# Kernel tuning notes

Measured on AMD Instinct MI355X. Metric: run time of the kernel, lower is better.

## Reference

```python
import jax, jax.numpy as jnp
import numpy as np

EMBEDDING_DIM = 256
NUM_EMBEDDINGS = 2048
COMMITMENT_COST = 0.25


def setup_inputs() -> dict:
    key = jax.random.key(0)
    k1, k2 = jax.random.split(key)
    inputs = jax.random.normal(k1, (32, EMBEDDING_DIM, 32, 32), dtype=jnp.float32)
    # learned codebook buffer, shape (D, K) as in the torch module
    embedding = jax.random.normal(k2, (EMBEDDING_DIM, NUM_EMBEDDINGS), dtype=jnp.float32)
    return {"inputs": inputs, "embedding": embedding}


def reference(inputs, embedding):
    # Eval-mode forward of VectorQuantizerEMA (EMA buffer updates are
    # training-only side effects and do not affect the returned values).
    B, D, H, W = inputs.shape
    K = embedding.shape[1]
    x = inputs.astype(jnp.float32)
    # (B, D, H, W) -> (N, D), N = B*H*W, clamped as in the source
    flat = jnp.clip(jnp.transpose(x, (0, 2, 3, 1)).reshape(-1, D), -10.0, 10.0)
    # squared L2 distances to every codeword: (N, K)
    distances = (
        jnp.sum(flat * flat, axis=1, keepdims=True)
        + jnp.sum(embedding * embedding, axis=0, keepdims=True)
        - 2.0 * (flat @ embedding)
    )
    encoding_indices = jnp.argmin(distances, axis=1)  # (N,)
    # one-hot @ emb.T is just a gather of codebook columns
    q_flat = jnp.take(embedding.T, encoding_indices, axis=0)  # (N, D)
    quantized = jnp.transpose(q_flat.reshape(B, H, W, D), (0, 3, 1, 2))
    # VQ losses (computed against the un-clamped float inputs, as in torch)
    e_latent_loss = jnp.mean((jax.lax.stop_gradient(quantized) - x) ** 2)
    q_latent_loss = jnp.mean((quantized - jax.lax.stop_gradient(x)) ** 2)
    loss = q_latent_loss + COMMITMENT_COST * e_latent_loss
    # straight-through estimator
    quantized_st = inputs + jax.lax.stop_gradient(quantized - inputs)
    # perplexity from codeword usage (mean one-hot == normalized counts)
    n = encoding_indices.shape[0]
    avg_probs = jnp.zeros((K,), dtype=jnp.float32).at[encoding_indices].add(1.0) / n
    perplexity = jnp.exp(-jnp.sum(avg_probs * jnp.log(avg_probs + 1e-10)))
    return quantized_st, loss, perplexity, encoding_indices
```

## Files before the change

### kernel.cpp

```cpp
#include <hip/hip_runtime.h>
#include <hip/hip_bf16.h>
#include <math.h>

typedef unsigned int  uint;
typedef unsigned short ushort;

#define DD    256
#define KK    2048
#define HW    1024
#define NN    32768
#define NUMEL 8388608
#define STRIDEB (DD*HW)
#define NBLK_QL (NUMEL/1024)

#define WS_H2     0
#define WS_COUNTS 8192
#define WS_LOSS   16384
#define WS_EBF    16512
#define WS_PV     2113664
#define WS_PI     2375808
#define WS_BPART  WS_PV

#define OUT_LOSS  8388608
#define OUT_PPL   8388609
#define OUT_IDX   8388610

typedef __attribute__((ext_vector_type(8))) short  short8;
typedef __attribute__((ext_vector_type(4))) float  float4v;

__device__ __forceinline__ ushort f2bf(float f) {
    uint u = __float_as_uint(f);
    return (ushort)((u + 0x7FFFu + ((u >> 16) & 1u)) >> 16);
}

__global__ __launch_bounds__(256) void e2h_kernel(const float* __restrict__ emb,
                                                  float* __restrict__ h2,
                                                  int*   __restrict__ counts) {
    int k = blockIdx.x * 256 + threadIdx.x;
    float s = 0.f;
    for (int d = 0; d < DD; ++d) {
        float v = emb[(size_t)d * KK + k];
        s += v * v;
    }
    h2[k] = 0.5f * s;
    counts[k] = 0;
}

__global__ __launch_bounds__(256) void prep_emb(const float* __restrict__ emb,
                                                ushort* __restrict__ ebf) {
    int g  = blockIdx.x * 256 + threadIdx.x;
    int k  = g & (KK - 1);
    int dg = g >> 11;
    int d0 = dg * 8;
    int s    = dg >> 2;
    int quad = dg & 3;
    int ct   = k >> 4;
    int l    = quad * 16 + (k & 15);

    union { ushort us[8]; uint4 v; } hu, lu;
#pragma unroll
    for (int j = 0; j < 8; ++j) {
        float v = emb[(size_t)(d0 + j) * KK + k];
        ushort hb = f2bf(v);
        float  hf = __uint_as_float(((uint)hb) << 16);
        hu.us[j] = hb;
        lu.us[j] = f2bf(v - hf);
    }
    size_t hi_off = (size_t)(((ct * 8 + s) * 2 + 0) * 64 + l) * 8;
    size_t lo_off = (size_t)(((ct * 8 + s) * 2 + 1) * 64 + l) * 8;
    *(uint4*)(ebf + hi_off) = hu.v;
    *(uint4*)(ebf + lo_off) = lu.v;
}

__global__ __launch_bounds__(256, 2) void argmin_mfma(
    const float*  __restrict__ x,
    const ushort* __restrict__ ebf,
    const float*  __restrict__ h2,
    float* __restrict__ pv,
    int*   __restrict__ pi)
{
    __shared__ ushort sB[8192];

    const int tid  = threadIdx.x;
    const int w    = tid >> 6;
    const int lane = tid & 63;
    const int m    = lane & 15;
    const int quad = lane >> 4;

    const int rb = blockIdx.x >> 1;
    const int ch = blockIdx.x & 1;
    const int n0 = rb * 128 + w * 32;
    const int b  = n0 >> 10;
    const int hwb = n0 & 1023;
    const float* xb = x + (size_t)b * STRIDEB;

    short8 xh[2][8], xl[2][8];
#pragma unroll
    for (int st = 0; st < 2; ++st) {
        const int hw = hwb + st * 16 + m;
#pragma unroll
        for (int s = 0; s < 8; ++s) {
            const float* p = xb + (size_t)(s * 32 + quad * 8) * HW + hw;
            short8 hh, ll;
#pragma unroll
            for (int j = 0; j < 8; ++j) {
                float v = p[(size_t)j * HW];
                v = fminf(fmaxf(v, -10.f), 10.f);
                ushort hb = f2bf(v);
                float  hf = __uint_as_float(((uint)hb) << 16);
                hh[j] = (short)hb;
                ll[j] = (short)f2bf(v - hf);
            }
            xh[st][s] = hh;
            xl[st][s] = ll;
        }
    }

    float bv[2][4] = {{1e30f,1e30f,1e30f,1e30f},{1e30f,1e30f,1e30f,1e30f}};
    int   bi[2][4] = {{0,0,0,0},{0,0,0,0}};
    const int cbase = ch * 1024;

    for (int ct = 0; ct < 64; ++ct) {
        const int ctg = (cbase >> 4) + ct;
        __syncthreads();
        {
            const uint4* gsrc = (const uint4*)(ebf + (size_t)ctg * 8192);
            uint4* ldst = (uint4*)sB;
#pragma unroll
            for (int i = 0; i < 4; ++i) ldst[tid + i * 256] = gsrc[tid + i * 256];
        }
        __syncthreads();

        float4v ahh0 = {0,0,0,0}, ahl0 = {0,0,0,0}, alh0 = {0,0,0,0};
        float4v ahh1 = {0,0,0,0}, ahl1 = {0,0,0,0}, alh1 = {0,0,0,0};
#pragma unroll
        for (int s = 0; s < 8; ++s) {
            short8 eh = *(const short8*)&sB[(s * 2 + 0) * 512 + lane * 8];
            short8 el = *(const short8*)&sB[(s * 2 + 1) * 512 + lane * 8];
            alh0 = __builtin_amdgcn_mfma_f32_16x16x32_bf16(xl[0][s], eh, alh0, 0, 0, 0);
            ahl0 = __builtin_amdgcn_mfma_f32_16x16x32_bf16(xh[0][s], el, ahl0, 0, 0, 0);
            ahh0 = __builtin_amdgcn_mfma_f32_16x16x32_bf16(xh[0][s], eh, ahh0, 0, 0, 0);
            alh1 = __builtin_amdgcn_mfma_f32_16x16x32_bf16(xl[1][s], eh, alh1, 0, 0, 0);
            ahl1 = __builtin_amdgcn_mfma_f32_16x16x32_bf16(xh[1][s], el, ahl1, 0, 0, 0);
            ahh1 = __builtin_amdgcn_mfma_f32_16x16x32_bf16(xh[1][s], eh, ahh1, 0, 0, 0);
        }
        const int c  = cbase + ct * 16 + m;
        const float hv = h2[c];
#pragma unroll
        for (int i = 0; i < 4; ++i) {
            float s0 = hv - (ahh0[i] + (ahl0[i] + alh0[i]));
            float s1 = hv - (ahh1[i] + (ahl1[i] + alh1[i]));
            if (s0 < bv[0][i]) { bv[0][i] = s0; bi[0][i] = c; }
            if (s1 < bv[1][i]) { bv[1][i] = s1; bi[1][i] = c; }
        }
    }

#pragma unroll
    for (int st = 0; st < 2; ++st) {
#pragma unroll
        for (int i = 0; i < 4; ++i) {
            float v  = bv[st][i];
            int   ix = bi[st][i];
#pragma unroll
            for (int msk = 8; msk >= 1; msk >>= 1) {
                float ov = __shfl_xor(v, msk, 64);
                int   oi = __shfl_xor(ix, msk, 64);
                if (ov < v || (ov == v && oi < ix)) { v = ov; ix = oi; }
            }
            if (m == 0) {
                int n = n0 + st * 16 + quad * 4 + i;
                pv[n * 2 + ch] = v;
                pi[n * 2 + ch] = ix;
            }
        }
    }
}

__global__ __launch_bounds__(256) void merge_kernel(
    const float* __restrict__ pv, const int* __restrict__ pi,
    float* __restrict__ out_idx_f, int* __restrict__ counts)
{
    int n = blockIdx.x * 256 + threadIdx.x;
    float v0 = pv[n * 2 + 0], v1 = pv[n * 2 + 1];
    int   i0 = pi[n * 2 + 0], i1 = pi[n * 2 + 1];
    int ix = (v1 < v0) ? i1 : i0;
    ix = min(max(ix, 0), KK - 1);
    out_idx_f[n] = (float)ix;
    atomicAdd(&counts[ix], 1);
}

__global__ __launch_bounds__(256) void quant_loss_kernel(
    const float* __restrict__ x,
    const float* __restrict__ emb,
    const float* __restrict__ idxf,
    float* __restrict__ outq,
    float* __restrict__ bpart)
{
    __shared__ float red[4];
    size_t o4 = ((size_t)blockIdx.x * 256 + threadIdx.x) * 4;
    int b  = (int)(o4 >> 18);
    int d  = (int)((o4 >> 10) & 255);
    int n  = b * HW + (int)(o4 & 1023);
    int i0 = (int)idxf[n + 0];
    int i1 = (int)idxf[n + 1];
    int i2 = (int)idxf[n + 2];
    int i3 = (int)idxf[n + 3];
    i0 = min(max(i0, 0), KK - 1); i1 = min(max(i1, 0), KK - 1);
    i2 = min(max(i2, 0), KK - 1); i3 = min(max(i3, 0), KK - 1);
    const float* er = emb + (size_t)d * KK;
    float4 q;
    q.x = er[i0]; q.y = er[i1]; q.z = er[i2]; q.w = er[i3];
    const float4 xv = *(const float4*)(x + o4);
    *(float4*)(outq + o4) = q;
    float ax = q.x - xv.x, ay = q.y - xv.y, az = q.z - xv.z, aw = q.w - xv.w;
    float s = ax * ax + ay * ay + az * az + aw * aw;
#pragma unroll
    for (int off = 32; off > 0; off >>= 1) s += __shfl_down(s, off, 64);
    if ((threadIdx.x & 63) == 0) red[threadIdx.x >> 6] = s;
    __syncthreads();
    if (threadIdx.x == 0)
        bpart[blockIdx.x] = red[0] + red[1] + red[2] + red[3];
}

__global__ __launch_bounds__(256) void finalize_kernel(
    const int* __restrict__ counts,
    const float* __restrict__ bpart,
    float* __restrict__ out)
{
    __shared__ float redp[4], redl[4];
    int tid = threadIdx.x;
    float s = 0.f;
    for (int k = tid; k < KK; k += 256) {
        float p = (float)counts[k] * (1.0f / (float)NN);
        s += p * logf(p + 1e-10f);
    }
    float ls = 0.f;
    for (int k = tid; k < NBLK_QL; k += 256) ls += bpart[k];
#pragma unroll
    for (int off = 32; off > 0; off >>= 1) {
        s  += __shfl_down(s, off, 64);
        ls += __shfl_down(ls, off, 64);
    }
    if ((tid & 63) == 0) { redp[tid >> 6] = s; redl[tid >> 6] = ls; }
    __syncthreads();
    if (tid == 0) {
        float tot = redp[0] + redp[1] + redp[2] + redp[3];
        float lsum = redl[0] + redl[1] + redl[2] + redl[3];
        out[OUT_PPL]  = expf(-tot);
        out[OUT_LOSS] = lsum * 1.25f / (float)NUMEL;
    }
}

extern "C" void kernel_launch(void* const* d_in, const int* in_sizes, int n_in,
                              void* d_out, int out_size, void* d_ws, size_t ws_size,
                              hipStream_t stream) {
    const float* x   = (const float*)d_in[0];
    const float* emb = (const float*)d_in[1];
    float* out = (float*)d_out;
    char*  ws  = (char*)d_ws;

    float*  h2     = (float*)(ws + WS_H2);
    int*    counts = (int*)(ws + WS_COUNTS);
    ushort* ebf    = (ushort*)(ws + WS_EBF);
    float*  pv     = (float*)(ws + WS_PV);
    int*    pi     = (int*)(ws + WS_PI);
    float*  bpart  = (float*)(ws + WS_BPART);

    e2h_kernel<<<KK / 256, 256, 0, stream>>>(emb, h2, counts);
    prep_emb<<<256, 256, 0, stream>>>(emb, ebf);
    argmin_mfma<<<512, 256, 0, stream>>>(x, ebf, h2, pv, pi);
    merge_kernel<<<NN / 256, 256, 0, stream>>>(pv, pi, out + OUT_IDX, counts);
    quant_loss_kernel<<<NBLK_QL, 256, 0, stream>>>(x, emb, out + OUT_IDX, out, bpart);
    finalize_kernel<<<1, 256, 0, stream>>>(counts, bpart, out);
}
```

Before: 233.0 us.

## Double-buffer codebook tiles in LDS with async global_load_lds and stage h2

```diff
diff --git a/kernel.cpp b/kernel.cpp
--- a/kernel.cpp
+++ b/kernel.cpp
@@ -27,6 +27,9 @@
 
 typedef __attribute__((ext_vector_type(8))) short  short8;
 typedef __attribute__((ext_vector_type(4))) float  float4v;
+
+typedef __attribute__((address_space(1))) uint guint;
+typedef __attribute__((address_space(3))) uint luint;
 
 __device__ __forceinline__ ushort f2bf(float f) {
     uint u = __float_as_uint(f);
@@ -79,7 +82,8 @@
     float* __restrict__ pv,
     int*   __restrict__ pi)
 {
-    __shared__ ushort sB[8192];
+    __shared__ ushort sB[2][8192];
+    __shared__ float  sH2[1024];
 
     const int tid  = threadIdx.x;
     const int w    = tid >> 6;
@@ -93,6 +97,21 @@
     const int b  = n0 >> 10;
     const int hwb = n0 & 1023;
     const float* xb = x + (size_t)b * STRIDEB;
+    const int cbase = ch * 1024;
+    const int ctg0  = cbase >> 4;
+
+    auto stage = [&](ushort* dst, int ctg) {
+        const char* gs = (const char*)(ebf + (size_t)ctg * 8192) + tid * 16;
+        char*       ls = (char*)dst + tid * 16;
+#pragma unroll
+        for (int i = 0; i < 4; ++i)
+            __builtin_amdgcn_global_load_lds((guint*)(gs + i * 4096),
+                                             (luint*)(ls + i * 4096),
+                                             16, 0, 0);
+    };
+
+    stage(sB[0], ctg0);
+    ((float4*)sH2)[tid] = ((const float4*)(h2 + cbase))[tid];
 
     short8 xh[2][8], xl[2][8];
 #pragma unroll
@@ -118,25 +137,14 @@
 
     float bv[2][4] = {{1e30f,1e30f,1e30f,1e30f},{1e30f,1e30f,1e30f,1e30f}};
     int   bi[2][4] = {{0,0,0,0},{0,0,0,0}};
-    const int cbase = ch * 1024;
-
-    for (int ct = 0; ct < 64; ++ct) {
-        const int ctg = (cbase >> 4) + ct;
-        __syncthreads();
-        {
-            const uint4* gsrc = (const uint4*)(ebf + (size_t)ctg * 8192);
-            uint4* ldst = (uint4*)sB;
-#pragma unroll
-            for (int i = 0; i < 4; ++i) ldst[tid + i * 256] = gsrc[tid + i * 256];
-        }
-        __syncthreads();
-
+
+    auto compute_tile = [&](const ushort* sbc, int ct) {
         float4v ahh0 = {0,0,0,0}, ahl0 = {0,0,0,0}, alh0 = {0,0,0,0};
         float4v ahh1 = {0,0,0,0}, ahl1 = {0,0,0,0}, alh1 = {0,0,0,0};
 #pragma unroll
         for (int s = 0; s < 8; ++s) {
-            short8 eh = *(const short8*)&sB[(s * 2 + 0) * 512 + lane * 8];
-            short8 el = *(const short8*)&sB[(s * 2 + 1) * 512 + lane * 8];
+            short8 eh = *(const short8*)&sbc[(s * 2 + 0) * 512 + lane * 8];
+            short8 el = *(const short8*)&sbc[(s * 2 + 1) * 512 + lane * 8];
             alh0 = __builtin_amdgcn_mfma_f32_16x16x32_bf16(xl[0][s], eh, alh0, 0, 0, 0);
             ahl0 = __builtin_amdgcn_mfma_f32_16x16x32_bf16(xh[0][s], el, ahl0, 0, 0, 0);
             ahh0 = __builtin_amdgcn_mfma_f32_16x16x32_bf16(xh[0][s], eh, ahh0, 0, 0, 0);
@@ -145,7 +153,7 @@
             ahh1 = __builtin_amdgcn_mfma_f32_16x16x32_bf16(xh[1][s], eh, ahh1, 0, 0, 0);
         }
         const int c  = cbase + ct * 16 + m;
-        const float hv = h2[c];
+        const float hv = sH2[ct * 16 + m];
 #pragma unroll
         for (int i = 0; i < 4; ++i) {
             float s0 = hv - (ahh0[i] + (ahl0[i] + alh0[i]));
@@ -153,6 +161,17 @@
             if (s0 < bv[0][i]) { bv[0][i] = s0; bi[0][i] = c; }
             if (s1 < bv[1][i]) { bv[1][i] = s1; bi[1][i] = c; }
         }
+    };
+
+    __syncthreads();
+
+    for (int ct = 0; ct < 64; ct += 2) {
+        stage(sB[1], ctg0 + ct + 1);
+        compute_tile(sB[0], ct);
+        __syncthreads();
+        stage(sB[0], (ct + 2 < 64) ? (ctg0 + ct + 2) : ctg0);
+        compute_tile(sB[1], ct + 1);
+        __syncthreads();
     }
 
 #pragma unroll
```

Measured after the change: 226.7 us. 1.03x faster.

## Stream codebook fragments from global per wave and fuse argmin merge

Applied to the files above, without the earlier changes.

```diff
diff --git a/kernel.cpp b/kernel.cpp
--- a/kernel.cpp
+++ b/kernel.cpp
@@ -15,11 +15,8 @@
 
 #define WS_H2     0
 #define WS_COUNTS 8192
-#define WS_LOSS   16384
 #define WS_EBF    16512
-#define WS_PV     2113664
-#define WS_PI     2375808
-#define WS_BPART  WS_PV
+#define WS_BPART  2113664
 
 #define OUT_LOSS  8388608
 #define OUT_PPL   8388609
@@ -76,21 +73,17 @@
     const float*  __restrict__ x,
     const ushort* __restrict__ ebf,
     const float*  __restrict__ h2,
-    float* __restrict__ pv,
-    int*   __restrict__ pi)
+    float* __restrict__ out_idx_f,
+    int*   __restrict__ counts)
 {
-    __shared__ ushort sB[8192];
-
     const int tid  = threadIdx.x;
     const int w    = tid >> 6;
     const int lane = tid & 63;
     const int m    = lane & 15;
     const int quad = lane >> 4;
 
-    const int rb = blockIdx.x >> 1;
-    const int ch = blockIdx.x & 1;
-    const int n0 = rb * 128 + w * 32;
-    const int b  = n0 >> 10;
+    const int n0  = blockIdx.x * 128 + w * 32;
+    const int b   = n0 >> 10;
     const int hwb = n0 & 1023;
     const float* xb = x + (size_t)b * STRIDEB;
 
@@ -118,34 +111,30 @@
 
     float bv[2][4] = {{1e30f,1e30f,1e30f,1e30f},{1e30f,1e30f,1e30f,1e30f}};
     int   bi[2][4] = {{0,0,0,0},{0,0,0,0}};
-    const int cbase = ch * 1024;
-
-    for (int ct = 0; ct < 64; ++ct) {
-        const int ctg = (cbase >> 4) + ct;
-        __syncthreads();
-        {
-            const uint4* gsrc = (const uint4*)(ebf + (size_t)ctg * 8192);
-            uint4* ldst = (uint4*)sB;
-#pragma unroll
-            for (int i = 0; i < 4; ++i) ldst[tid + i * 256] = gsrc[tid + i * 256];
-        }
-        __syncthreads();
+
+    const short8* fp = (const short8*)ebf + lane;
+
+    for (int ct = 0; ct < 128; ++ct) {
+        short8 eh[8], el[8];
+#pragma unroll
+        for (int s = 0; s < 8; ++s) {
+            eh[s] = fp[(s * 2 + 0) * 64];
+            el[s] = fp[(s * 2 + 1) * 64];
+        }
+        const float hv = h2[ct * 16 + m];
 
         float4v ahh0 = {0,0,0,0}, ahl0 = {0,0,0,0}, alh0 = {0,0,0,0};
         float4v ahh1 = {0,0,0,0}, ahl1 = {0,0,0,0}, alh1 = {0,0,0,0};
 #pragma unroll
         for (int s = 0; s < 8; ++s) {
-            short8 eh = *(const short8*)&sB[(s * 2 + 0) * 512 + lane * 8];
-            short8 el = *(const short8*)&sB[(s * 2 + 1) * 512 + lane * 8];
-            alh0 = __builtin_amdgcn_mfma_f32_16x16x32_bf16(xl[0][s], eh, alh0, 0, 0, 0);
-            ahl0 = __builtin_amdgcn_mfma_f32_16x16x32_bf16(xh[0][s], el, ahl0, 0, 0, 0);
-            ahh0 = __builtin_amdgcn_mfma_f32_16x16x32_bf16(xh[0][s], eh, ahh0, 0, 0, 0);
-            alh1 = __builtin_amdgcn_mfma_f32_16x16x32_bf16(xl[1][s], eh, alh1, 0, 0, 0);
-            ahl1 = __builtin_amdgcn_mfma_f32_16x16x32_bf16(xh[1][s], el, ahl1, 0, 0, 0);
-            ahh1 = __builtin_amdgcn_mfma_f32_16x16x32_bf16(xh[1][s], eh, ahh1, 0, 0, 0);
-        }
-        const int c  = cbase + ct * 16 + m;
-        const float hv = h2[c];
+            alh0 = __builtin_amdgcn_mfma_f32_16x16x32_bf16(xl[0][s], eh[s], alh0, 0, 0, 0);
+            ahl0 = __builtin_amdgcn_mfma_f32_16x16x32_bf16(xh[0][s], el[s], ahl0, 0, 0, 0);
+            ahh0 = __builtin_amdgcn_mfma_f32_16x16x32_bf16(xh[0][s], eh[s], ahh0, 0, 0, 0);
+            alh1 = __builtin_amdgcn_mfma_f32_16x16x32_bf16(xl[1][s], eh[s], alh1, 0, 0, 0);
+            ahl1 = __builtin_amdgcn_mfma_f32_16x16x32_bf16(xh[1][s], el[s], ahl1, 0, 0, 0);
+            ahh1 = __builtin_amdgcn_mfma_f32_16x16x32_bf16(xh[1][s], eh[s], ahh1, 0, 0, 0);
+        }
+        const int c = ct * 16 + m;
 #pragma unroll
         for (int i = 0; i < 4; ++i) {
             float s0 = hv - (ahh0[i] + (ahl0[i] + alh0[i]));
@@ -153,6 +142,7 @@
             if (s0 < bv[0][i]) { bv[0][i] = s0; bi[0][i] = c; }
             if (s1 < bv[1][i]) { bv[1][i] = s1; bi[1][i] = c; }
         }
+        fp += 1024;
     }
 
 #pragma unroll
@@ -169,24 +159,12 @@
             }
             if (m == 0) {
                 int n = n0 + st * 16 + quad * 4 + i;
-                pv[n * 2 + ch] = v;
-                pi[n * 2 + ch] = ix;
+                ix = min(max(ix, 0), KK - 1);
+                out_idx_f[n] = (float)ix;
+                atomicAdd(&counts[ix], 1);
             }
         }
     }
-}
-
-__global__ __launch_bounds__(256) void merge_kernel(
-    const float* __restrict__ pv, const int* __restrict__ pi,
-    float* __restrict__ out_idx_f, int* __restrict__ counts)
-{
-    int n = blockIdx.x * 256 + threadIdx.x;
-    float v0 = pv[n * 2 + 0], v1 = pv[n * 2 + 1];
-    int   i0 = pi[n * 2 + 0], i1 = pi[n * 2 + 1];
-    int ix = (v1 < v0) ? i1 : i0;
-    ix = min(max(ix, 0), KK - 1);
-    out_idx_f[n] = (float)ix;
-    atomicAdd(&counts[ix], 1);
 }
 
 __global__ __launch_bounds__(256) void quant_loss_kernel(
@@ -262,14 +240,11 @@
     float*  h2     = (float*)(ws + WS_H2);
     int*    counts = (int*)(ws + WS_COUNTS);
     ushort* ebf    = (ushort*)(ws + WS_EBF);
-    float*  pv     = (float*)(ws + WS_PV);
-    int*    pi     = (int*)(ws + WS_PI);
     float*  bpart  = (float*)(ws + WS_BPART);
 
     e2h_kernel<<<KK / 256, 256, 0, stream>>>(emb, h2, counts);
     prep_emb<<<256, 256, 0, stream>>>(emb, ebf);
-    argmin_mfma<<<512, 256, 0, stream>>>(x, ebf, h2, pv, pi);
-    merge_kernel<<<NN / 256, 256, 0, stream>>>(pv, pi, out + OUT_IDX, counts);
+    argmin_mfma<<<NN / 128, 256, 0, stream>>>(x, ebf, h2, out + OUT_IDX, counts);
     quant_loss_kernel<<<NBLK_QL, 256, 0, stream>>>(x, emb, out + OUT_IDX, out, bpart);
     finalize_kernel<<<1, 256, 0, stream>>>(counts, bpart, out);
 }
```

Result: slower. 344.3 us (+47.8%).
